# Kernel tuning notes

Measured on AMD Instinct MI355X. Metric: run time of the kernel, lower is better.

## Reference

```python
import jax, jax.numpy as jnp
import numpy as np

EMBED_DIM = 256
NUM_HEADS = 8
HEAD_DIM = EMBED_DIM // NUM_HEADS
SCALE = HEAD_DIM ** (-0.5)
L, B = 2048, 2


def setup_inputs() -> dict:
    key = jax.random.key(0)
    ks = jax.random.split(key, 12)
    s = EMBED_DIM ** (-0.5)
    return {
        "query": jax.random.normal(ks[0], (L, B, EMBED_DIM), jnp.float32),
        "key_": jax.random.normal(ks[1], (L, B, EMBED_DIM), jnp.float32),
        "value": jax.random.normal(ks[2], (L, B, EMBED_DIM), jnp.float32),
        "Wq": jax.random.normal(ks[3], (EMBED_DIM, EMBED_DIM), jnp.float32) * s,
        "bq": jnp.zeros((EMBED_DIM,), jnp.float32),
        "Wk": jax.random.normal(ks[4], (EMBED_DIM, EMBED_DIM), jnp.float32) * s,
        "bk": jnp.zeros((EMBED_DIM,), jnp.float32),
        "Wv": jax.random.normal(ks[5], (EMBED_DIM, EMBED_DIM), jnp.float32) * s,
        "bv": jnp.zeros((EMBED_DIM,), jnp.float32),
        "Wp": jax.random.normal(ks[6], (EMBED_DIM, EMBED_DIM), jnp.float32) * s,
        "bp": jnp.zeros((EMBED_DIM,), jnp.float32),
    }


def reference(query, key_, value, Wq, bq, Wk, bk, Wv, bv, Wp, bp):
    # Inputs are seq-first: [L, B, E]. Dropout treated as eval (identity).
    Lq, Bq, E = query.shape
    q = (query @ Wq + bq).reshape(Lq, Bq, NUM_HEADS, HEAD_DIM)
    k = (key_ @ Wk + bk).reshape(key_.shape[0], Bq, NUM_HEADS, HEAD_DIM)
    v = (value @ Wv + bv).reshape(value.shape[0], Bq, NUM_HEADS, HEAD_DIM)
    # scores: [B, H, Lq, Lk]
    attn = jnp.einsum('qbhd,kbhd->bhqk', q, k) * SCALE
    attn = jax.nn.softmax(attn, axis=-1)
    out = jnp.einsum('bhqk,kbhd->qbhd', attn, v).reshape(Lq, Bq, E)
    return out @ Wp + bp
```

## Files before the change

### kernel.cpp

```cpp
#include <hip/hip_runtime.h>
#include <math.h>

#define L_SEQ 2048
#define BATCH 2
#define EMB   256
#define NH    8
#define HD    32
#define NROW  (L_SEQ * BATCH)
#define SCALE 0.17677669529663687f
#define LOG2E 1.4426950408889634f

typedef __attribute__((ext_vector_type(8))) short          short8;
typedef __attribute__((ext_vector_type(8))) unsigned short ushort8v;
typedef __attribute__((ext_vector_type(4))) unsigned short ushort4v;
typedef __attribute__((ext_vector_type(4))) float          floatx4;
typedef __attribute__((ext_vector_type(4))) unsigned int   uint4v;
typedef __attribute__((ext_vector_type(2))) unsigned int   uint2v;

__device__ __forceinline__ unsigned short f2b(float x) {
    unsigned int u = __float_as_uint(x);
    unsigned int r = u + 0x7FFFu + ((u >> 16) & 1u);
    return (unsigned short)(r >> 16);
}

__device__ __forceinline__ float b2f(unsigned short u) {
    return __uint_as_float(((unsigned int)u) << 16);
}

__device__ __forceinline__ unsigned int pk_bf16(float lo, float hi) {
    unsigned int ulo = __float_as_uint(lo);
    unsigned int uhi = __float_as_uint(hi);
    ulo += 0x7FFFu + ((ulo >> 16) & 1u);
    uhi += 0x7FFFu + ((uhi >> 16) & 1u);
    return __builtin_amdgcn_perm(uhi, ulo, 0x07060302);
}

__device__ __forceinline__ void pl16_swap(unsigned int& a, unsigned int& b) {
#if __has_builtin(__builtin_amdgcn_permlane16_swap)
    uint2v r = __builtin_amdgcn_permlane16_swap(a, b, false, false);
    a = r[0]; b = r[1];
#else
    asm volatile("v_permlane16_swap_b32 %0, %1" : "+v"(a), "+v"(b));
#endif
}

__device__ __forceinline__ float hw_exp2(float x) {
    return __builtin_amdgcn_exp2f(x);
}

__global__ __launch_bounds__(256) void wtrans_kernel(const float* __restrict__ Wq,
                                                     const float* __restrict__ Wk,
                                                     const float* __restrict__ Wv,
                                                     const float* __restrict__ Wp,
                                                     unsigned short* __restrict__ out) {
    __shared__ unsigned short T[64][65];
    const int wsel = blockIdx.z;
    const float* W = (wsel == 0) ? Wq : (wsel == 1) ? Wk : (wsel == 2) ? Wv : Wp;
    const float scale = (wsel == 0) ? (SCALE * LOG2E) : 1.0f;
    unsigned short* dst = out + (size_t)wsel * EMB * EMB;
    const int k0 = blockIdx.x * 64, n0 = blockIdx.y * 64;
    const int tid = threadIdx.x;

    #pragma unroll
    for (int i = 0; i < 4; ++i) {
        int idx = tid + 256 * i;
        int r = idx >> 4, c4 = (idx & 15) * 4;
        float4 f = *(const float4*)&W[(size_t)(k0 + r) * EMB + n0 + c4];
        T[r][c4 + 0] = f2b(f.x * scale);
        T[r][c4 + 1] = f2b(f.y * scale);
        T[r][c4 + 2] = f2b(f.z * scale);
        T[r][c4 + 3] = f2b(f.w * scale);
    }
    __syncthreads();
    #pragma unroll
    for (int i = 0; i < 4; ++i) {
        int idx = tid + 256 * i;
        int rn = idx >> 4, ck = (idx & 15) * 4;
        ushort4v p;
        #pragma unroll
        for (int j = 0; j < 4; ++j) p[j] = T[ck + j][rn];
        *(ushort4v*)&dst[(size_t)(n0 + rn) * EMB + k0 + ck] = p;
    }
}

__global__ __launch_bounds__(256) void qkv_proj(const float* __restrict__ Xq,
                                                const float* __restrict__ Xk,
                                                const float* __restrict__ Xv,
                                                const unsigned short* __restrict__ Wt,
                                                const float* __restrict__ bq,
                                                const float* __restrict__ bk,
                                                const float* __restrict__ bv,
                                                unsigned short* __restrict__ outq,
                                                unsigned short* __restrict__ outk,
                                                unsigned short* __restrict__ outvt) {
    __shared__ unsigned short Xs[64][136];
    __shared__ unsigned short Ws[64][136];
    const int z = blockIdx.z;
    const float* X    = (z == 0) ? Xq : (z == 1) ? Xk : Xv;
    const float* bias = (z == 0) ? bq : (z == 1) ? bk : bv;
    const float bscale = (z == 0) ? (SCALE * LOG2E) : 1.0f;
    const unsigned short* W = Wt + (size_t)z * EMB * EMB;

    const int row0 = blockIdx.x * 64;
    const int col0 = blockIdx.y * 64;
    const int tid  = threadIdx.x;
    const int w    = tid >> 6;
    const int lane = tid & 63;
    const int l16  = lane & 15;
    const int quad = lane >> 4;
    const floatx4 zero4 = {0.f, 0.f, 0.f, 0.f};

    floatx4 acc[4] = {zero4, zero4, zero4, zero4};

    #pragma unroll
    for (int kh = 0; kh < 2; ++kh) {
        if (kh) __syncthreads();
        #pragma unroll
        for (int i = 0; i < 4; ++i) {
            int idx = tid + 256 * i;
            int r = idx >> 4, c8 = (idx & 15) * 8;
            const float4* xp = (const float4*)&X[(size_t)(row0 + r) * EMB + kh * 128 + c8];
            float4 f0 = xp[0], f1 = xp[1];
            uint4 pk;
            pk.x = pk_bf16(f0.x, f0.y); pk.y = pk_bf16(f0.z, f0.w);
            pk.z = pk_bf16(f1.x, f1.y); pk.w = pk_bf16(f1.z, f1.w);
            *(uint4*)&Xs[r][c8] = pk;
            *(ushort8v*)&Ws[r][c8] =
                *(const ushort8v*)&W[(size_t)(col0 + r) * EMB + kh * 128 + c8];
        }
        __syncthreads();

        #pragma unroll
        for (int k = 0; k < 128; k += 32) {
            short8 a = *(const short8*)&Xs[w * 16 + l16][k + quad * 8];
            #pragma unroll
            for (int g = 0; g < 4; ++g) {
                short8 bf = *(const short8*)&Ws[g * 16 + l16][k + quad * 8];
                acc[g] = __builtin_amdgcn_mfma_f32_16x16x32_bf16(a, bf, acc[g], 0, 0, 0);
            }
        }
    }

    if (z == 2) {
        __syncthreads();
        #pragma unroll
        for (int g = 0; g < 4; ++g) {
            int n = g * 16 + l16;
            float bb = bias[col0 + n] * bscale;
            #pragma unroll
            for (int r = 0; r < 4; ++r)
                Xs[w * 16 + quad * 4 + r][n] = f2b(acc[g][r] + bb);
        }
        __syncthreads();
        #pragma unroll
        for (int i = 0; i < 2; ++i) {
            int idx = tid + 256 * i;
            int n = idx >> 3, sub = idx & 7;
            int bb2 = sub >> 2, lq = sub & 3;
            ushort8v p;
            #pragma unroll
            for (int j = 0; j < 8; ++j) p[j] = Xs[(lq * 8 + j) * 2 + bb2][n];
            int h = (col0 + n) >> 5, d = (col0 + n) & 31;
            size_t base = ((size_t)(bb2 * NH + h) * HD + d) * L_SEQ + (row0 >> 1) + lq * 8;
            *(ushort8v*)&outvt[base] = p;
        }
    } else {
        unsigned short* outp = z ? outk : outq;
        #pragma unroll
        for (int g = 0; g < 4; ++g) {
            int c = col0 + g * 16 + l16;
            float bb = bias[c] * bscale;
            #pragma unroll
            for (int r = 0; r < 4; ++r) {
                int rg = row0 + w * 16 + quad * 4 + r;
                int b = rg & 1, ll = rg >> 1;
                int h = c >> 5, d = c & 31;
                outp[(((size_t)(b * NH + h) * L_SEQ) + ll) * HD + d] = f2b(acc[g][r] + bb);
            }
        }
    }
}

__global__ __launch_bounds__(256) void attn_kernel(const unsigned short* __restrict__ Q,
                                                   const unsigned short* __restrict__ K,
                                                   const unsigned short* __restrict__ Vt,
                                                   unsigned short* __restrict__ Opart,
                                                   float* __restrict__ lpart) {
    __shared__ unsigned short Vs[2][32][136];

    const int tid  = threadIdx.x;
    const int w    = tid >> 6;
    const int lane = tid & 63;
    const int l16  = lane & 15;
    const int quad = lane >> 4;
    const int qs   = ((quad & 1) << 1) | (quad >> 1);

    const int l0   = blockIdx.x * 64;
    const int h    = blockIdx.y;
    const int b    = blockIdx.z & 1;
    const int half = blockIdx.z >> 1;
    const int koff = half * (L_SEQ / 2);
    const size_t bh = (size_t)(b * NH + h);

    const unsigned short* Qg  = Q  + (bh * L_SEQ) * HD;
    const unsigned short* Kg  = K  + (bh * L_SEQ + koff) * HD;
    const unsigned short* Vtg = Vt + (bh * HD) * L_SEQ + koff;

    short8 qfrag = *(const short8*)&Qg[(size_t)(l0 + w * 16 + l16) * HD + quad * 8];

    float lacc = 0.0f;
    const floatx4 zero4 = {0.f, 0.f, 0.f, 0.f};
    floatx4 o0 = zero4, o1 = zero4;

    const int vd = tid >> 3;
    const int vj = (tid & 7) * 8;

    short8 kf[8];
    #pragma unroll
    for (int g = 0; g < 8; ++g)
        kf[g] = *(const short8*)&Kg[(size_t)(g * 16 + l16) * HD + quad * 8];

    *(ushort8v*)&Vs[0][vd][vj]      = *(const ushort8v*)&Vtg[(size_t)vd * L_SEQ + vj];
    *(ushort8v*)&Vs[0][vd][64 + vj] = *(const ushort8v*)&Vtg[(size_t)vd * L_SEQ + 64 + vj];

    const int NT = (L_SEQ / 2) / 128;
    for (int kt = 0; kt < NT; ++kt) {
        floatx4 s[8];
        #pragma unroll
        for (int g = 0; g < 8; ++g)
            s[g] = __builtin_amdgcn_mfma_f32_16x16x32_bf16(kf[g], qfrag, zero4, 0, 0, 0);

        __syncthreads();

        ushort8v vn0, vn1;
        if (kt + 1 < NT) {
            #pragma unroll
            for (int g = 0; g < 8; ++g)
                kf[g] = *(const short8*)
                    &Kg[(size_t)((kt + 1) * 128 + g * 16 + l16) * HD + quad * 8];
            vn0 = *(const ushort8v*)&Vtg[(size_t)vd * L_SEQ + (kt + 1) * 128 + vj];
            vn1 = *(const ushort8v*)&Vtg[(size_t)vd * L_SEQ + (kt + 1) * 128 + 64 + vj];
        }

        const unsigned short (*Vc)[136] = Vs[kt & 1];
        #pragma unroll
        for (int c = 0; c < 4; ++c) {
            float a0 = hw_exp2(s[2 * c][0]),     a1 = hw_exp2(s[2 * c][1]);
            float a2 = hw_exp2(s[2 * c][2]),     a3 = hw_exp2(s[2 * c][3]);
            float b0 = hw_exp2(s[2 * c + 1][0]), b1 = hw_exp2(s[2 * c + 1][1]);
            float b2 = hw_exp2(s[2 * c + 1][2]), b3 = hw_exp2(s[2 * c + 1][3]);
            lacc += ((a0 + a1) + (a2 + a3)) + ((b0 + b1) + (b2 + b3));
            unsigned int X  = pk_bf16(a0, a1);
            unsigned int X2 = pk_bf16(a2, a3);
            unsigned int Y  = pk_bf16(b0, b1);
            unsigned int Y2 = pk_bf16(b2, b3);
            pl16_swap(X, Y);
            pl16_swap(X2, Y2);
            uint4v pfu = {X, X2, Y, Y2};
            short8 pf = __builtin_bit_cast(short8, pfu);
            short8 va = *(const short8*)&Vc[l16][c * 32 + qs * 8];
            short8 vb = *(const short8*)&Vc[16 + l16][c * 32 + qs * 8];
            o0 = __builtin_amdgcn_mfma_f32_16x16x32_bf16(va, pf, o0, 0, 0, 0);
            o1 = __builtin_amdgcn_mfma_f32_16x16x32_bf16(vb, pf, o1, 0, 0, 0);
        }

        if (kt + 1 < NT) {
            *(ushort8v*)&Vs[(kt + 1) & 1][vd][vj]      = vn0;
            *(ushort8v*)&Vs[(kt + 1) & 1][vd][64 + vj] = vn1;
        }
    }

    lacc += __shfl_xor(lacc, 16);
    lacc += __shfl_xor(lacc, 32);

    int query = l0 + w * 16 + l16;
    if (lane < 16)
        lpart[(size_t)half * (BATCH * NH * L_SEQ) + bh * L_SEQ + query] = lacc;

    size_t base = (size_t)half * ((size_t)NROW * EMB) +
                  ((size_t)query * BATCH + b) * EMB + h * HD;
    uint2 e0, e1;
    e0.x = pk_bf16(o0[0], o0[1]);
    e0.y = pk_bf16(o0[2], o0[3]);
    e1.x = pk_bf16(o1[0], o1[1]);
    e1.y = pk_bf16(o1[2], o1[3]);
    *(uint2*)&Opart[base + quad * 4] = e0;
    *(uint2*)&Opart[base + 16 + quad * 4] = e1;
}

__global__ __launch_bounds__(256) void out_proj(const unsigned short* __restrict__ Opart,
                                                const float* __restrict__ lpart,
                                                const unsigned short* __restrict__ Wt,
                                                const float* __restrict__ bias,
                                                float* __restrict__ out) {
    __shared__ unsigned short Xs[32][264];
    __shared__ unsigned short Ws[32][264];
    const int row0 = blockIdx.x * 32;
    const int col0 = blockIdx.y * 32;
    const int tid  = threadIdx.x;
    const int w    = tid >> 6;
    const int rw   = (w & 1) * 16;
    const int cw   = (w >> 1) * 16;
    const int lane = tid & 63;
    const int l16  = lane & 15;
    const int quad = lane >> 4;

    const size_t OP = (size_t)NROW * EMB;
    const size_t LP = (size_t)BATCH * NH * L_SEQ;

    #pragma unroll
    for (int i = 0; i < 4; ++i) {
        int idx = tid + 256 * i;
        int r = idx >> 5, c8 = (idx & 31) * 8;
        int rg = row0 + r;
        int bb = rg & 1, q = rg >> 1, hh = c8 >> 5;
        size_t lidx = ((size_t)(bb * NH + hh)) * L_SEQ + q;
        float inv = __builtin_amdgcn_rcpf(lpart[lidx] + lpart[LP + lidx]);

        ushort8v u0 = *(const ushort8v*)&Opart[(size_t)rg * EMB + c8];
        ushort8v u1 = *(const ushort8v*)&Opart[OP + (size_t)rg * EMB + c8];
        uint4 pk;
        pk.x = pk_bf16((b2f(u0[0]) + b2f(u1[0])) * inv, (b2f(u0[1]) + b2f(u1[1])) * inv);
        pk.y = pk_bf16((b2f(u0[2]) + b2f(u1[2])) * inv, (b2f(u0[3]) + b2f(u1[3])) * inv);
        pk.z = pk_bf16((b2f(u0[4]) + b2f(u1[4])) * inv, (b2f(u0[5]) + b2f(u1[5])) * inv);
        pk.w = pk_bf16((b2f(u0[6]) + b2f(u1[6])) * inv, (b2f(u0[7]) + b2f(u1[7])) * inv);
        *(uint4*)&Xs[r][c8] = pk;

        *(ushort8v*)&Ws[r][c8] = *(const ushort8v*)&Wt[(size_t)(col0 + r) * EMB + c8];
    }
    __syncthreads();

    floatx4 acc = {0.f, 0.f, 0.f, 0.f};
    #pragma unroll
    for (int k = 0; k < EMB; k += 32) {
        short8 a  = *(const short8*)&Xs[rw + l16][k + quad * 8];
        short8 bf = *(const short8*)&Ws[cw + l16][k + quad * 8];
        acc = __builtin_amdgcn_mfma_f32_16x16x32_bf16(a, bf, acc, 0, 0, 0);
    }

    int c = col0 + cw + l16;
    float bb = bias[c];
    #pragma unroll
    for (int r = 0; r < 4; ++r) {
        int rg = row0 + rw + quad * 4 + r;
        out[(size_t)rg * EMB + c] = acc[r] + bb;
    }
}

extern "C" void kernel_launch(void* const* d_in, const int* in_sizes, int n_in,
                              void* d_out, int out_size, void* d_ws, size_t ws_size,
                              hipStream_t stream) {
    const float* query = (const float*)d_in[0];
    const float* key_  = (const float*)d_in[1];
    const float* value = (const float*)d_in[2];
    const float* Wq    = (const float*)d_in[3];
    const float* bq    = (const float*)d_in[4];
    const float* Wk    = (const float*)d_in[5];
    const float* bk    = (const float*)d_in[6];
    const float* Wv    = (const float*)d_in[7];
    const float* bv    = (const float*)d_in[8];
    const float* Wp    = (const float*)d_in[9];
    const float* bp    = (const float*)d_in[10];
    float* out = (float*)d_out;

    unsigned short* ws = (unsigned short*)d_ws;
    const size_t WSZ = (size_t)EMB * EMB;
    const size_t M   = (size_t)NROW * EMB;
    unsigned short* wt    = ws;
    unsigned short* qw    = ws + 4 * WSZ;
    unsigned short* kw    = qw + M;
    unsigned short* vtw   = kw + M;
    unsigned short* opart = vtw + M;
    float*          lpart = (float*)(opart + 2 * M);

    wtrans_kernel<<<dim3(4, 4, 4), 256, 0, stream>>>(Wq, Wk, Wv, Wp, wt);

    qkv_proj<<<dim3(NROW / 64, EMB / 64, 3), 256, 0, stream>>>(
        query, key_, value, wt, bq, bk, bv, qw, kw, vtw);

    attn_kernel<<<dim3(L_SEQ / 64, NH, BATCH * 2), 256, 0, stream>>>(
        qw, kw, vtw, opart, lpart);

    out_proj<<<dim3(NROW / 32, EMB / 32), 256, 0, stream>>>(
        opart, lpart, wt + 3 * WSZ, bp, out);
}
```

Measured before the change: 115.1 us.

## Fuse all four stages into one persistent kernel with software grid barriers

Replaces the four separate launches (weight transpose, QKV projection, attention, output projection) with a single persistent kernel of 512 blocks. The blocks loop over each stage's work items and meet at atomic-counter grid barriers between stages. The aim is to remove per-launch overhead and inter-kernel gaps. In exchange, correctness depends on all 512 blocks being co-resident, barrier spinning adds latency, and each stage loses the natural block count it had as a separate launch.

```diff
diff --git a/kernel.cpp b/kernel.cpp
--- a/kernel.cpp
+++ b/kernel.cpp
@@ -9,6 +9,7 @@
 #define NROW  (L_SEQ * BATCH)
 #define SCALE 0.17677669529663687f
 #define LOG2E 1.4426950408889634f
+#define GRID  512
 
 typedef __attribute__((ext_vector_type(8))) short          short8;
 typedef __attribute__((ext_vector_type(8))) unsigned short ushort8v;
@@ -48,61 +49,34 @@
     return __builtin_amdgcn_exp2f(x);
 }
 
-__global__ __launch_bounds__(256) void wtrans_kernel(const float* __restrict__ Wq,
-                                                     const float* __restrict__ Wk,
-                                                     const float* __restrict__ Wv,
-                                                     const float* __restrict__ Wp,
-                                                     unsigned short* __restrict__ out) {
-    __shared__ unsigned short T[64][65];
-    const int wsel = blockIdx.z;
-    const float* W = (wsel == 0) ? Wq : (wsel == 1) ? Wk : (wsel == 2) ? Wv : Wp;
-    const float scale = (wsel == 0) ? (SCALE * LOG2E) : 1.0f;
-    unsigned short* dst = out + (size_t)wsel * EMB * EMB;
-    const int k0 = blockIdx.x * 64, n0 = blockIdx.y * 64;
-    const int tid = threadIdx.x;
-
-    #pragma unroll
-    for (int i = 0; i < 4; ++i) {
-        int idx = tid + 256 * i;
-        int r = idx >> 4, c4 = (idx & 15) * 4;
-        float4 f = *(const float4*)&W[(size_t)(k0 + r) * EMB + n0 + c4];
-        T[r][c4 + 0] = f2b(f.x * scale);
-        T[r][c4 + 1] = f2b(f.y * scale);
-        T[r][c4 + 2] = f2b(f.z * scale);
-        T[r][c4 + 3] = f2b(f.w * scale);
-    }
+__device__ __forceinline__ void gridbar(unsigned int* cnt) {
     __syncthreads();
-    #pragma unroll
-    for (int i = 0; i < 4; ++i) {
-        int idx = tid + 256 * i;
-        int rn = idx >> 4, ck = (idx & 15) * 4;
-        ushort4v p;
-        #pragma unroll
-        for (int j = 0; j < 4; ++j) p[j] = T[ck + j][rn];
-        *(ushort4v*)&dst[(size_t)(n0 + rn) * EMB + k0 + ck] = p;
-    }
-}
-
-__global__ __launch_bounds__(256) void qkv_proj(const float* __restrict__ Xq,
-                                                const float* __restrict__ Xk,
-                                                const float* __restrict__ Xv,
-                                                const unsigned short* __restrict__ Wt,
-                                                const float* __restrict__ bq,
-                                                const float* __restrict__ bk,
-                                                const float* __restrict__ bv,
-                                                unsigned short* __restrict__ outq,
-                                                unsigned short* __restrict__ outk,
-                                                unsigned short* __restrict__ outvt) {
-    __shared__ unsigned short Xs[64][136];
-    __shared__ unsigned short Ws[64][136];
-    const int z = blockIdx.z;
-    const float* X    = (z == 0) ? Xq : (z == 1) ? Xk : Xv;
-    const float* bias = (z == 0) ? bq : (z == 1) ? bk : bv;
-    const float bscale = (z == 0) ? (SCALE * LOG2E) : 1.0f;
-    const unsigned short* W = Wt + (size_t)z * EMB * EMB;
-
-    const int row0 = blockIdx.x * 64;
-    const int col0 = blockIdx.y * 64;
+    if (threadIdx.x == 0) {
+        __threadfence();
+        atomicAdd(cnt, 1u);
+        while (atomicAdd(cnt, 0u) < GRID)
+            __builtin_amdgcn_s_sleep(2);
+        __threadfence();
+    }
+    __syncthreads();
+}
+
+__global__ __launch_bounds__(256, 2) void fused_kernel(
+    const float* __restrict__ Xq, const float* __restrict__ Xk,
+    const float* __restrict__ Xv,
+    const float* __restrict__ Wq, const float* __restrict__ bq,
+    const float* __restrict__ Wk, const float* __restrict__ bk,
+    const float* __restrict__ Wv, const float* __restrict__ bv,
+    const float* __restrict__ Wp, const float* __restrict__ bp,
+    unsigned short* __restrict__ wt,
+    unsigned short* __restrict__ qw, unsigned short* __restrict__ kw,
+    unsigned short* __restrict__ vtw, unsigned short* __restrict__ opart,
+    float* __restrict__ lpart, unsigned int* __restrict__ bar,
+    float* __restrict__ out)
+{
+    __shared__ __attribute__((aligned(16))) unsigned short S[2 * 64 * 136];
+
+    const int bid  = blockIdx.x;
     const int tid  = threadIdx.x;
     const int w    = tid >> 6;
     const int lane = tid & 63;
@@ -110,240 +84,283 @@
     const int quad = lane >> 4;
     const floatx4 zero4 = {0.f, 0.f, 0.f, 0.f};
 
-    floatx4 acc[4] = {zero4, zero4, zero4, zero4};
-
-    #pragma unroll
-    for (int kh = 0; kh < 2; ++kh) {
-        if (kh) __syncthreads();
+    if (bid < 64) {
+        auto T = (unsigned short (*)[65])S;
+        const int wsel = bid >> 4;
+        const int rem  = bid & 15;
+        const int k0 = (rem & 3) * 64, n0 = (rem >> 2) * 64;
+        const float* W = (wsel == 0) ? Wq : (wsel == 1) ? Wk : (wsel == 2) ? Wv : Wp;
+        const float scale = (wsel == 0) ? (SCALE * LOG2E) : 1.0f;
+        unsigned short* dst = wt + (size_t)wsel * EMB * EMB;
+
         #pragma unroll
         for (int i = 0; i < 4; ++i) {
             int idx = tid + 256 * i;
-            int r = idx >> 4, c8 = (idx & 15) * 8;
-            const float4* xp = (const float4*)&X[(size_t)(row0 + r) * EMB + kh * 128 + c8];
-            float4 f0 = xp[0], f1 = xp[1];
-            uint4 pk;
-            pk.x = pk_bf16(f0.x, f0.y); pk.y = pk_bf16(f0.z, f0.w);
-            pk.z = pk_bf16(f1.x, f1.y); pk.w = pk_bf16(f1.z, f1.w);
-            *(uint4*)&Xs[r][c8] = pk;
-            *(ushort8v*)&Ws[r][c8] =
-                *(const ushort8v*)&W[(size_t)(col0 + r) * EMB + kh * 128 + c8];
-        }
-        __syncthreads();
-
-        #pragma unroll
-        for (int k = 0; k < 128; k += 32) {
-            short8 a = *(const short8*)&Xs[w * 16 + l16][k + quad * 8];
-            #pragma unroll
-            for (int g = 0; g < 4; ++g) {
-                short8 bf = *(const short8*)&Ws[g * 16 + l16][k + quad * 8];
-                acc[g] = __builtin_amdgcn_mfma_f32_16x16x32_bf16(a, bf, acc[g], 0, 0, 0);
-            }
-        }
-    }
-
-    if (z == 2) {
+            int r = idx >> 4, c4 = (idx & 15) * 4;
+            float4 f = *(const float4*)&W[(size_t)(k0 + r) * EMB + n0 + c4];
+            T[r][c4 + 0] = f2b(f.x * scale);
+            T[r][c4 + 1] = f2b(f.y * scale);
+            T[r][c4 + 2] = f2b(f.z * scale);
+            T[r][c4 + 3] = f2b(f.w * scale);
+        }
         __syncthreads();
         #pragma unroll
-        for (int g = 0; g < 4; ++g) {
-            int n = g * 16 + l16;
-            float bb = bias[col0 + n] * bscale;
-            #pragma unroll
-            for (int r = 0; r < 4; ++r)
-                Xs[w * 16 + quad * 4 + r][n] = f2b(acc[g][r] + bb);
-        }
-        __syncthreads();
-        #pragma unroll
-        for (int i = 0; i < 2; ++i) {
+        for (int i = 0; i < 4; ++i) {
             int idx = tid + 256 * i;
-            int n = idx >> 3, sub = idx & 7;
-            int bb2 = sub >> 2, lq = sub & 3;
-            ushort8v p;
-            #pragma unroll
-            for (int j = 0; j < 8; ++j) p[j] = Xs[(lq * 8 + j) * 2 + bb2][n];
-            int h = (col0 + n) >> 5, d = (col0 + n) & 31;
-            size_t base = ((size_t)(bb2 * NH + h) * HD + d) * L_SEQ + (row0 >> 1) + lq * 8;
-            *(ushort8v*)&outvt[base] = p;
-        }
-    } else {
-        unsigned short* outp = z ? outk : outq;
-        #pragma unroll
-        for (int g = 0; g < 4; ++g) {
-            int c = col0 + g * 16 + l16;
-            float bb = bias[c] * bscale;
+            int rn = idx >> 4, ck = (idx & 15) * 4;
+            ushort4v p;
+            #pragma unroll
+            for (int j = 0; j < 4; ++j) p[j] = T[ck + j][rn];
+            *(ushort4v*)&dst[(size_t)(n0 + rn) * EMB + k0 + ck] = p;
+        }
+    }
+    gridbar(bar + 0);
+
+    {
+        auto Xs = (unsigned short (*)[136])S;
+        auto Ws = (unsigned short (*)[136])(S + 64 * 136);
+        for (int t = bid; t < 768; t += GRID) {
+            __syncthreads();
+            const int z = t >> 8, rem = t & 255;
+            const int row0 = (rem & 63) * 64;
+            const int col0 = (rem >> 6) * 64;
+            const float* X    = (z == 0) ? Xq : (z == 1) ? Xk : Xv;
+            const float* bias = (z == 0) ? bq : (z == 1) ? bk : bv;
+            const float bscale = (z == 0) ? (SCALE * LOG2E) : 1.0f;
+            const unsigned short* W = wt + (size_t)z * EMB * EMB;
+
+            floatx4 acc[4] = {zero4, zero4, zero4, zero4};
+
+            #pragma unroll
+            for (int kh = 0; kh < 2; ++kh) {
+                if (kh) __syncthreads();
+                #pragma unroll
+                for (int i = 0; i < 4; ++i) {
+                    int idx = tid + 256 * i;
+                    int r = idx >> 4, c8 = (idx & 15) * 8;
+                    const float4* xp =
+                        (const float4*)&X[(size_t)(row0 + r) * EMB + kh * 128 + c8];
+                    float4 f0 = xp[0], f1 = xp[1];
+                    uint4 pk;
+                    pk.x = pk_bf16(f0.x, f0.y); pk.y = pk_bf16(f0.z, f0.w);
+                    pk.z = pk_bf16(f1.x, f1.y); pk.w = pk_bf16(f1.z, f1.w);
+                    *(uint4*)&Xs[r][c8] = pk;
+                    *(ushort8v*)&Ws[r][c8] =
+                        *(const ushort8v*)&W[(size_t)(col0 + r) * EMB + kh * 128 + c8];
+                }
+                __syncthreads();
+
+                #pragma unroll
+                for (int k = 0; k < 128; k += 32) {
+                    short8 a = *(const short8*)&Xs[w * 16 + l16][k + quad * 8];
+                    #pragma unroll
+                    for (int g = 0; g < 4; ++g) {
+                        short8 bf = *(const short8*)&Ws[g * 16 + l16][k + quad * 8];
+                        acc[g] = __builtin_amdgcn_mfma_f32_16x16x32_bf16(a, bf, acc[g], 0, 0, 0);
+                    }
+                }
+            }
+
+            if (z == 2) {
+                __syncthreads();
+                #pragma unroll
+                for (int g = 0; g < 4; ++g) {
+                    int n = g * 16 + l16;
+                    float bb = bias[col0 + n] * bscale;
+                    #pragma unroll
+                    for (int r = 0; r < 4; ++r)
+                        Xs[w * 16 + quad * 4 + r][n] = f2b(acc[g][r] + bb);
+                }
+                __syncthreads();
+                #pragma unroll
+                for (int i = 0; i < 2; ++i) {
+                    int idx = tid + 256 * i;
+                    int n = idx >> 3, sub = idx & 7;
+                    int bb2 = sub >> 2, lq = sub & 3;
+                    ushort8v p;
+                    #pragma unroll
+                    for (int j = 0; j < 8; ++j) p[j] = Xs[(lq * 8 + j) * 2 + bb2][n];
+                    int h = (col0 + n) >> 5, d = (col0 + n) & 31;
+                    size_t base = ((size_t)(bb2 * NH + h) * HD + d) * L_SEQ +
+                                  (row0 >> 1) + lq * 8;
+                    *(ushort8v*)&vtw[base] = p;
+                }
+            } else {
+                unsigned short* outp = z ? kw : qw;
+                #pragma unroll
+                for (int g = 0; g < 4; ++g) {
+                    int c = col0 + g * 16 + l16;
+                    float bb = bias[c] * bscale;
+                    #pragma unroll
+                    for (int r = 0; r < 4; ++r) {
+                        int rg = row0 + w * 16 + quad * 4 + r;
+                        int b = rg & 1, ll = rg >> 1;
+                        int h = c >> 5, d = c & 31;
+                        outp[(((size_t)(b * NH + h) * L_SEQ) + ll) * HD + d] =
+                            f2b(acc[g][r] + bb);
+                    }
+                }
+            }
+        }
+    }
+    gridbar(bar + 1);
+
+    {
+        auto Vs = (unsigned short (*)[32][136])S;
+        const int qs = ((quad & 1) << 1) | (quad >> 1);
+
+        for (int t = bid; t < 1024; t += GRID) {
+            __syncthreads();
+            const int l0   = (t & 31) * 64;
+            const int h    = (t >> 5) & 7;
+            const int b    = (t >> 8) & 1;
+            const int half = t >> 9;
+            const int koff = half * (L_SEQ / 2);
+            const size_t bh = (size_t)(b * NH + h);
+
+            const unsigned short* Qg  = qw  + (bh * L_SEQ) * HD;
+            const unsigned short* Kg  = kw  + (bh * L_SEQ + koff) * HD;
+            const unsigned short* Vtg = vtw + (bh * HD) * L_SEQ + koff;
+
+            short8 qfrag = *(const short8*)&Qg[(size_t)(l0 + w * 16 + l16) * HD + quad * 8];
+
+            float lacc = 0.0f;
+            floatx4 o0 = zero4, o1 = zero4;
+
+            const int vd = tid >> 3;
+            const int vj = (tid & 7) * 8;
+
+            short8 kf[8];
+            #pragma unroll
+            for (int g = 0; g < 8; ++g)
+                kf[g] = *(const short8*)&Kg[(size_t)(g * 16 + l16) * HD + quad * 8];
+
+            *(ushort8v*)&Vs[0][vd][vj]      = *(const ushort8v*)&Vtg[(size_t)vd * L_SEQ + vj];
+            *(ushort8v*)&Vs[0][vd][64 + vj] = *(const ushort8v*)&Vtg[(size_t)vd * L_SEQ + 64 + vj];
+
+            const int NT = (L_SEQ / 2) / 128;
+            for (int kt = 0; kt < NT; ++kt) {
+                floatx4 s[8];
+                #pragma unroll
+                for (int g = 0; g < 8; ++g)
+                    s[g] = __builtin_amdgcn_mfma_f32_16x16x32_bf16(kf[g], qfrag, zero4, 0, 0, 0);
+
+                __syncthreads();
+
+                ushort8v vn0, vn1;
+                if (kt + 1 < NT) {
+                    #pragma unroll
+                    for (int g = 0; g < 8; ++g)
+                        kf[g] = *(const short8*)
+                            &Kg[(size_t)((kt + 1) * 128 + g * 16 + l16) * HD + quad * 8];
+                    vn0 = *(const ushort8v*)&Vtg[(size_t)vd * L_SEQ + (kt + 1) * 128 + vj];
+                    vn1 = *(const ushort8v*)&Vtg[(size_t)vd * L_SEQ + (kt + 1) * 128 + 64 + vj];
+                }
+
+                const unsigned short (*Vc)[136] = Vs[kt & 1];
+                #pragma unroll
+                for (int c = 0; c < 4; ++c) {
+                    float a0 = hw_exp2(s[2 * c][0]),     a1 = hw_exp2(s[2 * c][1]);
+                    float a2 = hw_exp2(s[2 * c][2]),     a3 = hw_exp2(s[2 * c][3]);
+                    float b0 = hw_exp2(s[2 * c + 1][0]), b1 = hw_exp2(s[2 * c + 1][1]);
+                    float b2 = hw_exp2(s[2 * c + 1][2]), b3 = hw_exp2(s[2 * c + 1][3]);
+                    lacc += ((a0 + a1) + (a2 + a3)) + ((b0 + b1) + (b2 + b3));
+                    unsigned int X  = pk_bf16(a0, a1);
+                    unsigned int X2 = pk_bf16(a2, a3);
+                    unsigned int Y  = pk_bf16(b0, b1);
+                    unsigned int Y2 = pk_bf16(b2, b3);
+                    pl16_swap(X, Y);
+                    pl16_swap(X2, Y2);
+                    uint4v pfu = {X, X2, Y, Y2};
+                    short8 pf = __builtin_bit_cast(short8, pfu);
+                    short8 va = *(const short8*)&Vc[l16][c * 32 + qs * 8];
+                    short8 vb = *(const short8*)&Vc[16 + l16][c * 32 + qs * 8];
+                    o0 = __builtin_amdgcn_mfma_f32_16x16x32_bf16(va, pf, o0, 0, 0, 0);
+                    o1 = __builtin_amdgcn_mfma_f32_16x16x32_bf16(vb, pf, o1, 0, 0, 0);
+                }
+
+                if (kt + 1 < NT) {
+                    *(ushort8v*)&Vs[(kt + 1) & 1][vd][vj]      = vn0;
+                    *(ushort8v*)&Vs[(kt + 1) & 1][vd][64 + vj] = vn1;
+                }
+            }
+
+            lacc += __shfl_xor(lacc, 16);
+            lacc += __shfl_xor(lacc, 32);
+
+            int query = l0 + w * 16 + l16;
+            if (lane < 16)
+                lpart[(size_t)half * (BATCH * NH * L_SEQ) + bh * L_SEQ + query] = lacc;
+
+            size_t base = (size_t)half * ((size_t)NROW * EMB) +
+                          ((size_t)query * BATCH + b) * EMB + h * HD;
+            uint2 e0, e1;
+            e0.x = pk_bf16(o0[0], o0[1]);
+            e0.y = pk_bf16(o0[2], o0[3]);
+            e1.x = pk_bf16(o1[0], o1[1]);
+            e1.y = pk_bf16(o1[2], o1[3]);
+            *(uint2*)&opart[base + quad * 4] = e0;
+            *(uint2*)&opart[base + 16 + quad * 4] = e1;
+        }
+    }
+    gridbar(bar + 2);
+
+    {
+        auto Xs = (unsigned short (*)[264])S;
+        auto Ws = (unsigned short (*)[264])(S + 32 * 264);
+        const int rw = (w & 1) * 16;
+        const int cw = (w >> 1) * 16;
+        const size_t OP = (size_t)NROW * EMB;
+        const size_t LP = (size_t)BATCH * NH * L_SEQ;
+        const unsigned short* Wtp = wt + 3 * (size_t)EMB * EMB;
+
+        for (int t = bid; t < 1024; t += GRID) {
+            __syncthreads();
+            const int row0 = (t & 127) * 32;
+            const int col0 = (t >> 7) * 32;
+
+            #pragma unroll
+            for (int i = 0; i < 4; ++i) {
+                int idx = tid + 256 * i;
+                int r = idx >> 5, c8 = (idx & 31) * 8;
+                int rg = row0 + r;
+                int bb = rg & 1, q = rg >> 1, hh = c8 >> 5;
+                size_t lidx = ((size_t)(bb * NH + hh)) * L_SEQ + q;
+                float inv = __builtin_amdgcn_rcpf(lpart[lidx] + lpart[LP + lidx]);
+
+                ushort8v u0 = *(const ushort8v*)&opart[(size_t)rg * EMB + c8];
+                ushort8v u1 = *(const ushort8v*)&opart[OP + (size_t)rg * EMB + c8];
+                uint4 pk;
+                pk.x = pk_bf16((b2f(u0[0]) + b2f(u1[0])) * inv,
+                               (b2f(u0[1]) + b2f(u1[1])) * inv);
+                pk.y = pk_bf16((b2f(u0[2]) + b2f(u1[2])) * inv,
+                               (b2f(u0[3]) + b2f(u1[3])) * inv);
+                pk.z = pk_bf16((b2f(u0[4]) + b2f(u1[4])) * inv,
+                               (b2f(u0[5]) + b2f(u1[5])) * inv);
+                pk.w = pk_bf16((b2f(u0[6]) + b2f(u1[6])) * inv,
+                               (b2f(u0[7]) + b2f(u1[7])) * inv);
+                *(uint4*)&Xs[r][c8] = pk;
+
+                *(ushort8v*)&Ws[r][c8] = *(const ushort8v*)&Wtp[(size_t)(col0 + r) * EMB + c8];
+            }
+            __syncthreads();
+
+            floatx4 acc = zero4;
+            #pragma unroll
+            for (int k = 0; k < EMB; k += 32) {
+                short8 a  = *(const short8*)&Xs[rw + l16][k + quad * 8];
+                short8 bf = *(const short8*)&Ws[cw + l16][k + quad * 8];
+                acc = __builtin_amdgcn_mfma_f32_16x16x32_bf16(a, bf, acc, 0, 0, 0);
+            }
+
+            int c = col0 + cw + l16;
+            float bb = bp[c];
             #pragma unroll
             for (int r = 0; r < 4; ++r) {
-                int rg = row0 + w * 16 + quad * 4 + r;
-                int b = rg & 1, ll = rg >> 1;
-                int h = c >> 5, d = c & 31;
-                outp[(((size_t)(b * NH + h) * L_SEQ) + ll) * HD + d] = f2b(acc[g][r] + bb);
-            }
-        }
-    }
-}
-
-__global__ __launch_bounds__(256) void attn_kernel(const unsigned short* __restrict__ Q,
-                                                   const unsigned short* __restrict__ K,
-                                                   const unsigned short* __restrict__ Vt,
-                                                   unsigned short* __restrict__ Opart,
-                                                   float* __restrict__ lpart) {
-    __shared__ unsigned short Vs[2][32][136];
-
-    const int tid  = threadIdx.x;
-    const int w    = tid >> 6;
-    const int lane = tid & 63;
-    const int l16  = lane & 15;
-    const int quad = lane >> 4;
-    const int qs   = ((quad & 1) << 1) | (quad >> 1);
-
-    const int l0   = blockIdx.x * 64;
-    const int h    = blockIdx.y;
-    const int b    = blockIdx.z & 1;
-    const int half = blockIdx.z >> 1;
-    const int koff = half * (L_SEQ / 2);
-    const size_t bh = (size_t)(b * NH + h);
-
-    const unsigned short* Qg  = Q  + (bh * L_SEQ) * HD;
-    const unsigned short* Kg  = K  + (bh * L_SEQ + koff) * HD;
-    const unsigned short* Vtg = Vt + (bh * HD) * L_SEQ + koff;
-
-    short8 qfrag = *(const short8*)&Qg[(size_t)(l0 + w * 16 + l16) * HD + quad * 8];
-
-    float lacc = 0.0f;
-    const floatx4 zero4 = {0.f, 0.f, 0.f, 0.f};
-    floatx4 o0 = zero4, o1 = zero4;
-
-    const int vd = tid >> 3;
-    const int vj = (tid & 7) * 8;
-
-    short8 kf[8];
-    #pragma unroll
-    for (int g = 0; g < 8; ++g)
-        kf[g] = *(const short8*)&Kg[(size_t)(g * 16 + l16) * HD + quad * 8];
-
-    *(ushort8v*)&Vs[0][vd][vj]      = *(const ushort8v*)&Vtg[(size_t)vd * L_SEQ + vj];
-    *(ushort8v*)&Vs[0][vd][64 + vj] = *(const ushort8v*)&Vtg[(size_t)vd * L_SEQ + 64 + vj];
-
-    const int NT = (L_SEQ / 2) / 128;
-    for (int kt = 0; kt < NT; ++kt) {
-        floatx4 s[8];
-        #pragma unroll
-        for (int g = 0; g < 8; ++g)
-            s[g] = __builtin_amdgcn_mfma_f32_16x16x32_bf16(kf[g], qfrag, zero4, 0, 0, 0);
-
-        __syncthreads();
-
-        ushort8v vn0, vn1;
-        if (kt + 1 < NT) {
-            #pragma unroll
-            for (int g = 0; g < 8; ++g)
-                kf[g] = *(const short8*)
-                    &Kg[(size_t)((kt + 1) * 128 + g * 16 + l16) * HD + quad * 8];
-            vn0 = *(const ushort8v*)&Vtg[(size_t)vd * L_SEQ + (kt + 1) * 128 + vj];
-            vn1 = *(const ushort8v*)&Vtg[(size_t)vd * L_SEQ + (kt + 1) * 128 + 64 + vj];
-        }
-
-        const unsigned short (*Vc)[136] = Vs[kt & 1];
-        #pragma unroll
-        for (int c = 0; c < 4; ++c) {
-            float a0 = hw_exp2(s[2 * c][0]),     a1 = hw_exp2(s[2 * c][1]);
-            float a2 = hw_exp2(s[2 * c][2]),     a3 = hw_exp2(s[2 * c][3]);
-            float b0 = hw_exp2(s[2 * c + 1][0]), b1 = hw_exp2(s[2 * c + 1][1]);
-            float b2 = hw_exp2(s[2 * c + 1][2]), b3 = hw_exp2(s[2 * c + 1][3]);
-            lacc += ((a0 + a1) + (a2 + a3)) + ((b0 + b1) + (b2 + b3));
-            unsigned int X  = pk_bf16(a0, a1);
-            unsigned int X2 = pk_bf16(a2, a3);
-            unsigned int Y  = pk_bf16(b0, b1);
-            unsigned int Y2 = pk_bf16(b2, b3);
-            pl16_swap(X, Y);
-            pl16_swap(X2, Y2);
-            uint4v pfu = {X, X2, Y, Y2};
-            short8 pf = __builtin_bit_cast(short8, pfu);
-            short8 va = *(const short8*)&Vc[l16][c * 32 + qs * 8];
-            short8 vb = *(const short8*)&Vc[16 + l16][c * 32 + qs * 8];
-            o0 = __builtin_amdgcn_mfma_f32_16x16x32_bf16(va, pf, o0, 0, 0, 0);
-            o1 = __builtin_amdgcn_mfma_f32_16x16x32_bf16(vb, pf, o1, 0, 0, 0);
-        }
-
-        if (kt + 1 < NT) {
-            *(ushort8v*)&Vs[(kt + 1) & 1][vd][vj]      = vn0;
-            *(ushort8v*)&Vs[(kt + 1) & 1][vd][64 + vj] = vn1;
-        }
-    }
-
-    lacc += __shfl_xor(lacc, 16);
-    lacc += __shfl_xor(lacc, 32);
-
-    int query = l0 + w * 16 + l16;
-    if (lane < 16)
-        lpart[(size_t)half * (BATCH * NH * L_SEQ) + bh * L_SEQ + query] = lacc;
-
-    size_t base = (size_t)half * ((size_t)NROW * EMB) +
-                  ((size_t)query * BATCH + b) * EMB + h * HD;
-    uint2 e0, e1;
-    e0.x = pk_bf16(o0[0], o0[1]);
-    e0.y = pk_bf16(o0[2], o0[3]);
-    e1.x = pk_bf16(o1[0], o1[1]);
-    e1.y = pk_bf16(o1[2], o1[3]);
-    *(uint2*)&Opart[base + quad * 4] = e0;
-    *(uint2*)&Opart[base + 16 + quad * 4] = e1;
-}
-
-__global__ __launch_bounds__(256) void out_proj(const unsigned short* __restrict__ Opart,
-                                                const float* __restrict__ lpart,
-                                                const unsigned short* __restrict__ Wt,
-                                                const float* __restrict__ bias,
-                                                float* __restrict__ out) {
-    __shared__ unsigned short Xs[32][264];
-    __shared__ unsigned short Ws[32][264];
-    const int row0 = blockIdx.x * 32;
-    const int col0 = blockIdx.y * 32;
-    const int tid  = threadIdx.x;
-    const int w    = tid >> 6;
-    const int rw   = (w & 1) * 16;
-    const int cw   = (w >> 1) * 16;
-    const int lane = tid & 63;
-    const int l16  = lane & 15;
-    const int quad = lane >> 4;
-
-    const size_t OP = (size_t)NROW * EMB;
-    const size_t LP = (size_t)BATCH * NH * L_SEQ;
-
-    #pragma unroll
-    for (int i = 0; i < 4; ++i) {
-        int idx = tid + 256 * i;
-        int r = idx >> 5, c8 = (idx & 31) * 8;
-        int rg = row0 + r;
-        int bb = rg & 1, q = rg >> 1, hh = c8 >> 5;
-        size_t lidx = ((size_t)(bb * NH + hh)) * L_SEQ + q;
-        float inv = __builtin_amdgcn_rcpf(lpart[lidx] + lpart[LP + lidx]);
-
-        ushort8v u0 = *(const ushort8v*)&Opart[(size_t)rg * EMB + c8];
-        ushort8v u1 = *(const ushort8v*)&Opart[OP + (size_t)rg * EMB + c8];
-        uint4 pk;
-        pk.x = pk_bf16((b2f(u0[0]) + b2f(u1[0])) * inv, (b2f(u0[1]) + b2f(u1[1])) * inv);
-        pk.y = pk_bf16((b2f(u0[2]) + b2f(u1[2])) * inv, (b2f(u0[3]) + b2f(u1[3])) * inv);
-        pk.z = pk_bf16((b2f(u0[4]) + b2f(u1[4])) * inv, (b2f(u0[5]) + b2f(u1[5])) * inv);
-        pk.w = pk_bf16((b2f(u0[6]) + b2f(u1[6])) * inv, (b2f(u0[7]) + b2f(u1[7])) * inv);
-        *(uint4*)&Xs[r][c8] = pk;
-
-        *(ushort8v*)&Ws[r][c8] = *(const ushort8v*)&Wt[(size_t)(col0 + r) * EMB + c8];
-    }
-    __syncthreads();
-
-    floatx4 acc = {0.f, 0.f, 0.f, 0.f};
-    #pragma unroll
-    for (int k = 0; k < EMB; k += 32) {
-        short8 a  = *(const short8*)&Xs[rw + l16][k + quad * 8];
-        short8 bf = *(const short8*)&Ws[cw + l16][k + quad * 8];
-        acc = __builtin_amdgcn_mfma_f32_16x16x32_bf16(a, bf, acc, 0, 0, 0);
-    }
-
-    int c = col0 + cw + l16;
-    float bb = bias[c];
-    #pragma unroll
-    for (int r = 0; r < 4; ++r) {
-        int rg = row0 + rw + quad * 4 + r;
-        out[(size_t)rg * EMB + c] = acc[r] + bb;
+                int rg = row0 + rw + quad * 4 + r;
+                out[(size_t)rg * EMB + c] = acc[r] + bb;
+            }
+        }
     }
 }
 
@@ -363,7 +380,8 @@
     const float* bp    = (const float*)d_in[10];
     float* out = (float*)d_out;
 
-    unsigned short* ws = (unsigned short*)d_ws;
+    unsigned int*   bar = (unsigned int*)d_ws;
+    unsigned short* ws  = (unsigned short*)d_ws + 32;
     const size_t WSZ = (size_t)EMB * EMB;
     const size_t M   = (size_t)NROW * EMB;
     unsigned short* wt    = ws;
@@ -373,14 +391,9 @@
     unsigned short* opart = vtw + M;
     float*          lpart = (float*)(opart + 2 * M);
 
-    wtrans_kernel<<<dim3(4, 4, 4), 256, 0, stream>>>(Wq, Wk, Wv, Wp, wt);
-
-    qkv_proj<<<dim3(NROW / 64, EMB / 64, 3), 256, 0, stream>>>(
-        query, key_, value, wt, bq, bk, bv, qw, kw, vtw);
-
-    attn_kernel<<<dim3(L_SEQ / 64, NH, BATCH * 2), 256, 0, stream>>>(
-        qw, kw, vtw, opart, lpart);
-
-    out_proj<<<dim3(NROW / 32, EMB / 32), 256, 0, stream>>>(
-        opart, lpart, wt + 3 * WSZ, bp, out);
-}
+    hipMemsetAsync(bar, 0, 64, stream);
+
+    fused_kernel<<<dim3(GRID), dim3(256), 0, stream>>>(
+        query, key_, value, Wq, bq, Wk, bk, Wv, bv, Wp, bp,
+        wt, qw, kw, vtw, opart, lpart, bar, out);
+}
```

After: 257.0 us. 123% more time.
